# Kernel optimization log

Measured on AMD Instinct MI355X. Metric: run time of the kernel, lower is better.

The kernel has to match this reference:

```python
import jax, jax.numpy as jnp
import numpy as np

N = 32768   # num nodes
E = 65536   # num edges
H = 64      # hidden_size
EH = 64     # edge_hidden_size
LN_EPS = 1e-5


def setup_inputs() -> dict:
    key = jax.random.key(0)
    ks = jax.random.split(key, 6)
    node_emb = jax.random.normal(ks[0], (N, H), dtype=jnp.float32)
    edge_emb = jax.random.normal(ks[1], (E, EH), dtype=jnp.float32)
    edge_index = jax.random.randint(ks[2], (2, E), 0, N, dtype=jnp.int64)
    # edge_weight_net MLP: edge_hidden -> hidden (relu) -> H*H, xavier-uniform style scales
    W1 = jax.random.normal(ks[3], (EH, H), dtype=jnp.float32) * (2.0 / (EH + H)) ** 0.5
    b1 = jnp.zeros((H,), dtype=jnp.float32)
    W2 = jax.random.normal(ks[4], (H, H * H), dtype=jnp.float32) * (2.0 / (H + H * H)) ** 0.5
    b2 = jnp.zeros((H * H,), dtype=jnp.float32)
    root = jax.random.normal(ks[5], (H, H), dtype=jnp.float32) * (2.0 / (H + H)) ** 0.5
    bias = jnp.zeros((H,), dtype=jnp.float32)
    gamma = jnp.ones((H,), dtype=jnp.float32)
    beta = jnp.zeros((H,), dtype=jnp.float32)
    return {"node_emb": node_emb, "edge_emb": edge_emb, "W1": W1, "b1": b1,
            "W2": W2, "b2": b2, "root": root, "bias": bias,
            "gamma": gamma, "beta": beta, "edge_index": edge_index}


def reference(node_emb, edge_emb, W1, b1, W2, b2, root, bias, gamma, beta, edge_index):
    src, dst = edge_index[0], edge_index[1]
    num_nodes = node_emb.shape[0]
    # edge-conditioned weight: MLP(edge_emb) -> per-edge [H, H] matrix ('full' mode)
    h = jax.nn.relu(edge_emb @ W1 + b1)                 # [E, H]
    W = (h @ W2 + b2).reshape(-1, H, H)                 # [E, H, H]
    # message = x_src @ W_e  (bmm of [1,H] x [H,H] per edge)
    msg = jnp.einsum('eh,ehk->ek', node_emb[src], W)    # [E, H]
    # scatter-add aggregation at destination nodes
    agg = jax.ops.segment_sum(msg, dst, num_segments=num_nodes)          # [N, H]
    deg = jax.ops.segment_sum(jnp.ones_like(dst, dtype=node_emb.dtype), dst,
                              num_segments=num_nodes)                    # [N]
    agg = agg / jnp.maximum(deg, 1.0)[:, None]          # 'mean' aggregation
    # root transform + bias + residual
    out = agg + node_emb @ root + bias + node_emb       # [N, H]
    # LayerNorm over hidden dim
    mu = jnp.mean(out, axis=-1, keepdims=True)
    var = jnp.var(out, axis=-1, keepdims=True)
    out = (out - mu) * jax.lax.rsqrt(var + LN_EPS) * gamma + beta
    return out
```

## Files before the change

kernel.cpp:

```cpp
#include <hip/hip_runtime.h>

#define N_NODES 32768
#define N_EDGES 65536

typedef _Float16 f16;
typedef _Float16 f16x8 __attribute__((ext_vector_type(8)));
typedef float f32x16 __attribute__((ext_vector_type(16)));
typedef unsigned int uint32;

#define WS_AGG   0
#define WS_DEG   8388608
#define WS_W2    8519680
#define WS_W1    9060352
#define WS_ROOT  9068544

#define MFMA(a, b, c) __builtin_amdgcn_mfma_f32_32x32x16_f16((a), (b), (c), 0, 0, 0)

__device__ inline f16 u16_as_f16(unsigned short u) {
  union { unsigned short s; f16 h; } v; v.s = u; return v.h;
}
__device__ inline f16x8 splat8(f16 x) {
  f16x8 r;
  #pragma unroll
  for (int u = 0; u < 8; ++u) r[u] = x;
  return r;
}
__device__ inline f16x8 cvt8(float4 p0, float4 p1) {
  f16x8 a;
  a[0] = (f16)p0.x; a[1] = (f16)p0.y; a[2] = (f16)p0.z; a[3] = (f16)p0.w;
  a[4] = (f16)p1.x; a[5] = (f16)p1.y; a[6] = (f16)p1.z; a[7] = (f16)p1.w;
  return a;
}

__global__ __launch_bounds__(256) void k_prep(const float* __restrict__ W1,
                                              const float* __restrict__ W2,
                                              const float* __restrict__ b2,
                                              const float* __restrict__ root,
                                              const int* __restrict__ eidx,
                                              float* __restrict__ deg,
                                              char* __restrict__ w2v2,
                                              char* __restrict__ w1v2,
                                              char* __restrict__ rootIv2) {
  int t = blockIdx.x * 256 + threadIdx.x;
  if (t < 65536) {
    int j = t >> 10, rem = t & 1023, h = rem >> 4, c4 = rem & 15;
    float4 v = *(const float4*)(W2 + j * 4096 + h * 64 + c4 * 4);
    int oct = j * 8 + (h >> 4) * 2 + ((h >> 3) & 1);
    char* base = w2v2 + oct * 1024 + (h & 7) * 2;
    *(f16*)(base + (c4 * 4 + 0) * 16) = (f16)v.x;
    *(f16*)(base + (c4 * 4 + 1) * 16) = (f16)v.y;
    *(f16*)(base + (c4 * 4 + 2) * 16) = (f16)v.z;
    *(f16*)(base + (c4 * 4 + 3) * 16) = (f16)v.w;
  } else if (t < 66560) {
    int u = t - 65536, h = u >> 4, c4 = u & 15;
    float4 v = *(const float4*)(b2 + h * 64 + c4 * 4);
    int oct = 512 + (h >> 4) * 2 + ((h >> 3) & 1);
    char* base = w2v2 + oct * 1024 + (h & 7) * 2;
    *(f16*)(base + (c4 * 4 + 0) * 16) = (f16)v.x;
    *(f16*)(base + (c4 * 4 + 1) * 16) = (f16)v.y;
    *(f16*)(base + (c4 * 4 + 2) * 16) = (f16)v.z;
    *(f16*)(base + (c4 * 4 + 3) * 16) = (f16)v.w;
  } else if (t < 67584) {
    int u = t - 66560, h = u >> 4, c4 = u & 15;
    int oct = 520 + (h >> 4) * 2 + ((h >> 3) & 1);
    char* base = w2v2 + oct * 1024 + (h & 7) * 2;
    #pragma unroll
    for (int q = 0; q < 4; ++q) *(f16*)(base + (c4 * 4 + q) * 16) = (f16)0.f;
  } else if (t < 68608) {
    int u = t - 67584, i = u >> 4, c4 = u & 15;
    float4 v = *(const float4*)(W1 + i * 64 + c4 * 4);
    int oct = (i >> 4) * 2 + ((i >> 3) & 1);
    char* base = w1v2 + oct * 1024 + (i & 7) * 2;
    *(f16*)(base + (c4 * 4 + 0) * 16) = (f16)v.x;
    *(f16*)(base + (c4 * 4 + 1) * 16) = (f16)v.y;
    *(f16*)(base + (c4 * 4 + 2) * 16) = (f16)v.z;
    *(f16*)(base + (c4 * 4 + 3) * 16) = (f16)v.w;
  } else if (t < 69632) {
    int u = t - 68608, i = u >> 4, c4 = u & 15;
    float4 v = *(const float4*)(root + i * 64 + c4 * 4);
    int oct = (i >> 4) * 2 + ((i >> 3) & 1);
    char* base = rootIv2 + oct * 1024 + (i & 7) * 2;
    *(f16*)(base + (c4 * 4 + 0) * 16) = (f16)(v.x + (i == c4 * 4 + 0 ? 1.f : 0.f));
    *(f16*)(base + (c4 * 4 + 1) * 16) = (f16)(v.y + (i == c4 * 4 + 1 ? 1.f : 0.f));
    *(f16*)(base + (c4 * 4 + 2) * 16) = (f16)(v.z + (i == c4 * 4 + 2 ? 1.f : 0.f));
    *(f16*)(base + (c4 * 4 + 3) * 16) = (f16)(v.w + (i == c4 * 4 + 3 ? 1.f : 0.f));
  } else if (t < 135168) {
    int e = t - 69632;
    unsafeAtomicAdd(&deg[eidx[N_EDGES + e]], 1.0f);
  }
}

__device__ inline void chunk_load(f16x8 (&buf)[8], const char* wp, int c) {
  #pragma unroll
  for (int jj = 0; jj < 2; ++jj)
    #pragma unroll
    for (int kk = 0; kk < 4; ++kk)
      buf[jj * 4 + kk] = *(const f16x8*)(wp + c * 16384 + ((jj * 8 + kk * 2) << 10));
}

__device__ inline void chunk_compute(const f16x8 (&buf)[8], uint32 hA, uint32 hB,
                                     const f16x8 (&xf)[2][4], f32x16 (&acc)[2]) {
  #pragma unroll
  for (int jj = 0; jj < 2; ++jj) {
    const f16x8 spA = splat8(u16_as_f16((unsigned short)(hA >> (jj * 16))));
    const f16x8 spB = splat8(u16_as_f16((unsigned short)(hB >> (jj * 16))));
    #pragma unroll
    for (int kk = 0; kk < 4; ++kk) {
      acc[0] = MFMA(xf[0][kk] * spA, buf[jj * 4 + kk], acc[0]);
      acc[1] = MFMA(xf[1][kk] * spB, buf[jj * 4 + kk], acc[1]);
    }
  }
}

__global__ __launch_bounds__(512, 2) void k_main(const float* __restrict__ node,
                                                 const float* __restrict__ edge,
                                                 const float* __restrict__ b1,
                                                 const int* __restrict__ eidx,
                                                 const char* __restrict__ w2v2,
                                                 const char* __restrict__ w1v2,
                                                 float* __restrict__ agg) {
  __shared__ char ldsH[34816];

  const int tid = threadIdx.x;
  const int lane = tid & 63;
  const int wv = tid >> 6;
  const int ln31 = lane & 31;
  const int half = lane >> 5;
  const int ebase = blockIdx.x * 256;

  {
    const char* w1p = w1v2 + half * 1024 + ln31 * 16;
    const int e = ebase + wv * 32 + ln31;
    const float4* er = (const float4*)edge + (long)e * 16;
    f32x16 c0 = {}, c1 = {};
    #pragma unroll
    for (int kk = 0; kk < 4; ++kk) {
      f16x8 a = cvt8(er[kk * 4 + half * 2], er[kk * 4 + half * 2 + 1]);
      f16x8 bf0 = *(const f16x8*)(w1p + (kk * 2 << 10));
      f16x8 bf1 = *(const f16x8*)(w1p + (kk * 2 << 10) + 512);
      c0 = MFMA(a, bf0, c0);
      c1 = MFMA(a, bf1, c1);
    }
    const float bb0 = b1[ln31], bb1 = b1[32 + ln31];
    char* hb = ldsH + wv * 32 * 136;
    #pragma unroll
    for (int r = 0; r < 16; ++r) {
      const int m = (r & 3) + 8 * (r >> 2) + 4 * half;
      *(f16*)(hb + m * 136 + ln31 * 2)      = (f16)fmaxf(c0[r] + bb0, 0.f);
      *(f16*)(hb + m * 136 + 64 + ln31 * 2) = (f16)fmaxf(c1[r] + bb1, 0.f);
    }
    if (half == 0)
      *(uint32*)(hb + ln31 * 136 + 128) = 0x00003C00u;
  }

  const int g = wv >> 1;
  const int ch = wv & 1;

  f16x8 xf[2][4];
  #pragma unroll
  for (int t = 0; t < 2; ++t) {
    const int e = ebase + (2 * g + t) * 32 + ln31;
    const int s = eidx[e];
    const float4* xr = (const float4*)node + (long)s * 16;
    #pragma unroll
    for (int kk = 0; kk < 4; ++kk)
      xf[t][kk] = cvt8(xr[kk * 4 + half * 2], xr[kk * 4 + half * 2 + 1]);
  }

  const char* wp = w2v2 + half * 1024 + ch * 512 + ln31 * 16;
  const char* hpA = ldsH + ((2 * g + 0) * 32 + ln31) * 136;
  const char* hpB = ldsH + ((2 * g + 1) * 32 + ln31) * 136;

  f16x8 b0[8], b1v[8];
  f32x16 acc[2] = {};
  chunk_load(b0, wp, 0);

  __syncthreads();

  for (int c = 0; c < 32; c += 2) {
    chunk_load(b1v, wp, c + 1);
    const uint32 hA0 = *(const uint32*)(hpA + c * 4);
    const uint32 hB0 = *(const uint32*)(hpB + c * 4);
    const uint32 hA1 = *(const uint32*)(hpA + c * 4 + 4);
    const uint32 hB1 = *(const uint32*)(hpB + c * 4 + 4);
    __builtin_amdgcn_s_setprio(1);
    chunk_compute(b0, hA0, hB0, xf, acc);
    __builtin_amdgcn_s_setprio(0);
    chunk_load(b0, wp, c + 2);
    __builtin_amdgcn_s_setprio(1);
    chunk_compute(b1v, hA1, hB1, xf, acc);
    __builtin_amdgcn_s_setprio(0);
  }
  {
    const uint32 hA = *(const uint32*)(hpA + 128);
    const uint32 hB = *(const uint32*)(hpB + 128);
    chunk_compute(b0, hA, hB, xf, acc);
  }

  #pragma unroll
  for (int t = 0; t < 2; ++t) {
    const int base_e = ebase + (2 * g + t) * 32;
    #pragma unroll
    for (int r = 0; r < 16; ++r) {
      const int m = (r & 3) + 8 * (r >> 2) + 4 * half;
      const int d = eidx[N_EDGES + base_e + m];
      unsafeAtomicAdd(&agg[(long)d * 64 + ch * 32 + ln31], acc[t][r]);
    }
  }
}

__global__ __launch_bounds__(256) void k_node(const float* __restrict__ node,
                                              const float* __restrict__ agg,
                                              const float* __restrict__ deg,
                                              const char* __restrict__ rootIv2,
                                              const float* __restrict__ bias,
                                              const float* __restrict__ gamma,
                                              const float* __restrict__ beta,
                                              float* __restrict__ out) {
  const int tid = threadIdx.x;
  const int lane = tid & 63;
  const int wv = tid >> 6;
  const int ln31 = lane & 31;
  const int half = lane >> 5;
  const int nb = blockIdx.x * 128 + wv * 32;

  const char* rp = rootIv2 + half * 1024 + ln31 * 16;
  f32x16 c0 = {}, c1 = {};
  const float4* xr = (const float4*)node + (long)(nb + ln31) * 16;
  #pragma unroll
  for (int kk = 0; kk < 4; ++kk) {
    f16x8 a = cvt8(xr[kk * 4 + half * 2], xr[kk * 4 + half * 2 + 1]);
    f16x8 b0 = *(const f16x8*)(rp + (kk * 2 << 10));
    f16x8 b1f = *(const f16x8*)(rp + (kk * 2 << 10) + 512);
    c0 = MFMA(a, b0, c0);
    c1 = MFMA(a, b1f, c1);
  }
  const float bi0 = bias[ln31],  bi1 = bias[32 + ln31];
  const float g0  = gamma[ln31], g1  = gamma[32 + ln31];
  const float be0 = beta[ln31],  be1 = beta[32 + ln31];
  #pragma unroll
  for (int r = 0; r < 16; ++r) {
    const int m = (r & 3) + 8 * (r >> 2) + 4 * half;
    const int n = nb + m;
    const float rd = 1.f / fmaxf(deg[n], 1.f);
    const float pre0 = agg[n * 64 + ln31] * rd + c0[r] + bi0;
    const float pre1 = agg[n * 64 + 32 + ln31] * rd + c1[r] + bi1;
    float s = pre0 + pre1, s2 = pre0 * pre0 + pre1 * pre1;
    #pragma unroll
    for (int mk = 16; mk >= 1; mk >>= 1) {
      s  += __shfl_xor(s, mk, 64);
      s2 += __shfl_xor(s2, mk, 64);
    }
    const float mu  = s * 0.015625f;
    const float var = s2 * 0.015625f - mu * mu;
    const float inv = rsqrtf(var + 1e-5f);
    out[n * 64 + ln31]      = (pre0 - mu) * inv * g0 + be0;
    out[n * 64 + 32 + ln31] = (pre1 - mu) * inv * g1 + be1;
  }
}

extern "C" void kernel_launch(void* const* d_in, const int* in_sizes, int n_in,
                              void* d_out, int out_size, void* d_ws, size_t ws_size,
                              hipStream_t stream) {
  const float* node  = (const float*)d_in[0];
  const float* edgee = (const float*)d_in[1];
  const float* W1    = (const float*)d_in[2];
  const float* b1    = (const float*)d_in[3];
  const float* W2    = (const float*)d_in[4];
  const float* b2    = (const float*)d_in[5];
  const float* root  = (const float*)d_in[6];
  const float* bias  = (const float*)d_in[7];
  const float* gamma = (const float*)d_in[8];
  const float* beta  = (const float*)d_in[9];
  const int*   eidx  = (const int*)d_in[10];
  float* out = (float*)d_out;

  char* ws = (char*)d_ws;
  float* agg     = (float*)(ws + WS_AGG);
  float* deg     = (float*)(ws + WS_DEG);
  char*  w2v2    = ws + WS_W2;
  char*  w1v2    = ws + WS_W1;
  char*  rootIv2 = ws + WS_ROOT;

  hipMemsetAsync(ws, 0, 8519680, stream);

  k_prep<<<528, 256, 0, stream>>>(W1, W2, b2, root, eidx, deg, w2v2, w1v2, rootIv2);
  k_main<<<256, 512, 0, stream>>>(node, edgee, b1, eidx, w2v2, w1v2, agg);
  k_node<<<256, 256, 0, stream>>>(node, agg, deg, rootIv2, bias, gamma, beta, out);
}
```

Measured before the change: 146.2 us.

## Stage W2 chunks into LDS via async global_load_lds with double buffering

The main kernel now streams each 16KB W2 chunk into a double-buffered LDS region using direct global-to-LDS loads shared by the whole block, instead of each wave loading its own copy of W2 into registers. Each block now handles 128 edges, with every wave owning one 32-edge tile and one half of the output columns, and the grid doubles to 512 blocks with launch bounds raised to 4 blocks per SM. The goal is to cut redundant L2 traffic and register pressure so occupancy can rise. In exchange there is a block-wide barrier on every chunk, and the W2 data reuse per wave is halved. The degree count also switches from float atomics to integer atomics.

New measurement: 146.6 us. Within noise of the previous version (+0.2%).

```diff
diff --git a/kernel.cpp b/kernel.cpp
--- a/kernel.cpp
+++ b/kernel.cpp
@@ -7,9 +7,11 @@
 typedef _Float16 f16x8 __attribute__((ext_vector_type(8)));
 typedef float f32x16 __attribute__((ext_vector_type(16)));
 typedef unsigned int uint32;
+typedef __attribute__((address_space(3))) void lds_t;
+typedef __attribute__((address_space(1))) void glb_t;
 
 #define WS_AGG   0
-#define WS_DEG   8388608
+#define WS_HIST  8388608
 #define WS_W2    8519680
 #define WS_W1    9060352
 #define WS_ROOT  9068544
@@ -37,7 +39,7 @@
                                               const float* __restrict__ b2,
                                               const float* __restrict__ root,
                                               const int* __restrict__ eidx,
-                                              float* __restrict__ deg,
+                                              int* __restrict__ hist,
                                               char* __restrict__ w2v2,
                                               char* __restrict__ w1v2,
                                               char* __restrict__ rootIv2) {
@@ -86,132 +88,118 @@
     *(f16*)(base + (c4 * 4 + 3) * 16) = (f16)(v.w + (i == c4 * 4 + 3 ? 1.f : 0.f));
   } else if (t < 135168) {
     int e = t - 69632;
-    unsafeAtomicAdd(&deg[eidx[N_EDGES + e]], 1.0f);
-  }
-}
-
-__device__ inline void chunk_load(f16x8 (&buf)[8], const char* wp, int c) {
-  #pragma unroll
-  for (int jj = 0; jj < 2; ++jj)
-    #pragma unroll
-    for (int kk = 0; kk < 4; ++kk)
-      buf[jj * 4 + kk] = *(const f16x8*)(wp + c * 16384 + ((jj * 8 + kk * 2) << 10));
-}
-
-__device__ inline void chunk_compute(const f16x8 (&buf)[8], uint32 hA, uint32 hB,
-                                     const f16x8 (&xf)[2][4], f32x16 (&acc)[2]) {
-  #pragma unroll
-  for (int jj = 0; jj < 2; ++jj) {
-    const f16x8 spA = splat8(u16_as_f16((unsigned short)(hA >> (jj * 16))));
-    const f16x8 spB = splat8(u16_as_f16((unsigned short)(hB >> (jj * 16))));
-    #pragma unroll
-    for (int kk = 0; kk < 4; ++kk) {
-      acc[0] = MFMA(xf[0][kk] * spA, buf[jj * 4 + kk], acc[0]);
-      acc[1] = MFMA(xf[1][kk] * spB, buf[jj * 4 + kk], acc[1]);
-    }
-  }
-}
-
-__global__ __launch_bounds__(512, 2) void k_main(const float* __restrict__ node,
+    atomicAdd(&hist[eidx[N_EDGES + e]], 1);
+  }
+}
+
+__global__ __launch_bounds__(512, 4) void k_main(const float* __restrict__ node,
                                                  const float* __restrict__ edge,
                                                  const float* __restrict__ b1,
                                                  const int* __restrict__ eidx,
                                                  const char* __restrict__ w2v2,
                                                  const char* __restrict__ w1v2,
                                                  float* __restrict__ agg) {
-  __shared__ char ldsH[34816];
-
+  __shared__ char smem[50176];
+
+  char* ldsH = smem + 32768;
   const int tid = threadIdx.x;
   const int lane = tid & 63;
   const int wv = tid >> 6;
   const int ln31 = lane & 31;
   const int half = lane >> 5;
-  const int ebase = blockIdx.x * 256;
-
-  {
-    const char* w1p = w1v2 + half * 1024 + ln31 * 16;
-    const int e = ebase + wv * 32 + ln31;
+  const int t = wv & 3;
+  const int ch = wv >> 2;
+  const int ebase = blockIdx.x * 128;
+
+  {
+    const int e = ebase + t * 32 + ln31;
     const float4* er = (const float4*)edge + (long)e * 16;
-    f32x16 c0 = {}, c1 = {};
+    f32x16 c0 = {};
     #pragma unroll
     for (int kk = 0; kk < 4; ++kk) {
       f16x8 a = cvt8(er[kk * 4 + half * 2], er[kk * 4 + half * 2 + 1]);
-      f16x8 bf0 = *(const f16x8*)(w1p + (kk * 2 << 10));
-      f16x8 bf1 = *(const f16x8*)(w1p + (kk * 2 << 10) + 512);
-      c0 = MFMA(a, bf0, c0);
-      c1 = MFMA(a, bf1, c1);
-    }
-    const float bb0 = b1[ln31], bb1 = b1[32 + ln31];
-    char* hb = ldsH + wv * 32 * 136;
+      f16x8 bf = *(const f16x8*)(w1v2 + (kk * 2 + half) * 1024 + ch * 512 + ln31 * 16);
+      c0 = MFMA(a, bf, c0);
+    }
+    const float bb = b1[ch * 32 + ln31];
+    char* hb = ldsH + t * 32 * 136;
     #pragma unroll
     for (int r = 0; r < 16; ++r) {
       const int m = (r & 3) + 8 * (r >> 2) + 4 * half;
-      *(f16*)(hb + m * 136 + ln31 * 2)      = (f16)fmaxf(c0[r] + bb0, 0.f);
-      *(f16*)(hb + m * 136 + 64 + ln31 * 2) = (f16)fmaxf(c1[r] + bb1, 0.f);
-    }
-    if (half == 0)
+      *(f16*)(hb + m * 136 + (ch * 32 + ln31) * 2) = (f16)fmaxf(c0[r] + bb, 0.f);
+    }
+    if (ch == 1)
       *(uint32*)(hb + ln31 * 136 + 128) = 0x00003C00u;
   }
 
-  const int g = wv >> 1;
-  const int ch = wv & 1;
-
-  f16x8 xf[2][4];
-  #pragma unroll
-  for (int t = 0; t < 2; ++t) {
-    const int e = ebase + (2 * g + t) * 32 + ln31;
+  f16x8 xf[4];
+  {
+    const int e = ebase + t * 32 + ln31;
     const int s = eidx[e];
     const float4* xr = (const float4*)node + (long)s * 16;
     #pragma unroll
     for (int kk = 0; kk < 4; ++kk)
-      xf[t][kk] = cvt8(xr[kk * 4 + half * 2], xr[kk * 4 + half * 2 + 1]);
-  }
-
-  const char* wp = w2v2 + half * 1024 + ch * 512 + ln31 * 16;
-  const char* hpA = ldsH + ((2 * g + 0) * 32 + ln31) * 136;
-  const char* hpB = ldsH + ((2 * g + 1) * 32 + ln31) * 136;
-
-  f16x8 b0[8], b1v[8];
-  f32x16 acc[2] = {};
-  chunk_load(b0, wp, 0);
-
-  __syncthreads();
-
-  for (int c = 0; c < 32; c += 2) {
-    chunk_load(b1v, wp, c + 1);
-    const uint32 hA0 = *(const uint32*)(hpA + c * 4);
-    const uint32 hB0 = *(const uint32*)(hpB + c * 4);
-    const uint32 hA1 = *(const uint32*)(hpA + c * 4 + 4);
-    const uint32 hB1 = *(const uint32*)(hpB + c * 4 + 4);
+      xf[kk] = cvt8(xr[kk * 4 + half * 2], xr[kk * 4 + half * 2 + 1]);
+  }
+
+  {
+    const char* s_ = w2v2 + tid * 16;
+    char* d_ = smem + tid * 16;
+    __builtin_amdgcn_global_load_lds((const glb_t*)s_, (lds_t*)d_, 16, 0, 0);
+    __builtin_amdgcn_global_load_lds((const glb_t*)(s_ + 8192), (lds_t*)(d_ + 8192), 16, 0, 0);
+  }
+
+  const char* hp = ldsH + (t * 32 + ln31) * 136;
+  f32x16 acc = {};
+
+  asm volatile("s_waitcnt vmcnt(0) lgkmcnt(0)" ::: "memory");
+  __builtin_amdgcn_sched_barrier(0);
+  __builtin_amdgcn_s_barrier();
+
+  int cur = 0;
+  #pragma unroll 1
+  for (int c = 0; c < 33; ++c) {
+    if (c < 32) {
+      const char* s_ = w2v2 + (c + 1) * 16384 + tid * 16;
+      char* d_ = smem + (cur ^ 1) * 16384 + tid * 16;
+      __builtin_amdgcn_global_load_lds((const glb_t*)s_, (lds_t*)d_, 16, 0, 0);
+      __builtin_amdgcn_global_load_lds((const glb_t*)(s_ + 8192), (lds_t*)(d_ + 8192), 16, 0, 0);
+    }
+    const uint32 hv = *(const uint32*)(hp + c * 4);
+    const char* bb_ = smem + cur * 16384 + half * 1024 + ch * 512 + ln31 * 16;
     __builtin_amdgcn_s_setprio(1);
-    chunk_compute(b0, hA0, hB0, xf, acc);
+    #pragma unroll
+    for (int jj = 0; jj < 2; ++jj) {
+      const f16x8 sp = splat8(u16_as_f16((unsigned short)(hv >> (jj * 16))));
+      #pragma unroll
+      for (int kk = 0; kk < 4; ++kk) {
+        const f16x8 B = *(const f16x8*)(bb_ + jj * 8192 + kk * 2048);
+        acc = MFMA(xf[kk] * sp, B, acc);
+      }
+    }
     __builtin_amdgcn_s_setprio(0);
-    chunk_load(b0, wp, c + 2);
-    __builtin_amdgcn_s_setprio(1);
-    chunk_compute(b1v, hA1, hB1, xf, acc);
-    __builtin_amdgcn_s_setprio(0);
-  }
-  {
-    const uint32 hA = *(const uint32*)(hpA + 128);
-    const uint32 hB = *(const uint32*)(hpB + 128);
-    chunk_compute(b0, hA, hB, xf, acc);
-  }
-
-  #pragma unroll
-  for (int t = 0; t < 2; ++t) {
-    const int base_e = ebase + (2 * g + t) * 32;
+    if (c < 32) {
+      asm volatile("s_waitcnt vmcnt(0)" ::: "memory");
+      __builtin_amdgcn_sched_barrier(0);
+      __builtin_amdgcn_s_barrier();
+      cur ^= 1;
+    }
+  }
+
+  {
+    const int base_e = ebase + t * 32;
     #pragma unroll
     for (int r = 0; r < 16; ++r) {
       const int m = (r & 3) + 8 * (r >> 2) + 4 * half;
       const int d = eidx[N_EDGES + base_e + m];
-      unsafeAtomicAdd(&agg[(long)d * 64 + ch * 32 + ln31], acc[t][r]);
+      unsafeAtomicAdd(&agg[(long)d * 64 + ch * 32 + ln31], acc[r]);
     }
   }
 }
 
 __global__ __launch_bounds__(256) void k_node(const float* __restrict__ node,
                                               const float* __restrict__ agg,
-                                              const float* __restrict__ deg,
+                                              const int* __restrict__ hist,
                                               const char* __restrict__ rootIv2,
                                               const float* __restrict__ bias,
                                               const float* __restrict__ gamma,
@@ -242,7 +230,7 @@
   for (int r = 0; r < 16; ++r) {
     const int m = (r & 3) + 8 * (r >> 2) + 4 * half;
     const int n = nb + m;
-    const float rd = 1.f / fmaxf(deg[n], 1.f);
+    const float rd = 1.f / fmaxf((float)hist[n], 1.f);
     const float pre0 = agg[n * 64 + ln31] * rd + c0[r] + bi0;
     const float pre1 = agg[n * 64 + 32 + ln31] * rd + c1[r] + bi1;
     float s = pre0 + pre1, s2 = pre0 * pre0 + pre1 * pre1;
@@ -277,14 +265,14 @@
 
   char* ws = (char*)d_ws;
   float* agg     = (float*)(ws + WS_AGG);
-  float* deg     = (float*)(ws + WS_DEG);
+  int*   hist    = (int*)(ws + WS_HIST);
   char*  w2v2    = ws + WS_W2;
   char*  w1v2    = ws + WS_W1;
   char*  rootIv2 = ws + WS_ROOT;
 
   hipMemsetAsync(ws, 0, 8519680, stream);
 
-  k_prep<<<528, 256, 0, stream>>>(W1, W2, b2, root, eidx, deg, w2v2, w1v2, rootIv2);
-  k_main<<<256, 512, 0, stream>>>(node, edgee, b1, eidx, w2v2, w1v2, agg);
-  k_node<<<256, 256, 0, stream>>>(node, agg, deg, rootIv2, bias, gamma, beta, out);
-}
+  k_prep<<<528, 256, 0, stream>>>(W1, W2, b2, root, eidx, hist, w2v2, w1v2, rootIv2);
+  k_main<<<512, 512, 0, stream>>>(node, edgee, b1, eidx, w2v2, w1v2, agg);
+  k_node<<<256, 256, 0, stream>>>(node, agg, hist, rootIv2, bias, gamma, beta, out);
+}
```
